# Kernel tuning notes

Hardware: AMD Instinct MI355X
Metric: run time of the kernel (lower is better)

The kernel has to match this reference:

```python
import jax, jax.numpy as jnp
import numpy as np

EMBED_DIM = 1024  # scaling uses embedding_dim**-0.5, as in the source
NEG_INF = -1e9    # keras Softmax masking constant


def setup_inputs() -> dict:
    key = jax.random.key(0)
    k0, k1, k2, k3 = jax.random.split(key, 4)
    B, S, D, H = 8, 2048, 1024, 128
    x = jax.random.normal(k0, (B, S, D), dtype=jnp.float32)
    Wq = jax.random.normal(k1, (D, H), dtype=jnp.float32) * (D ** -0.5)
    Wk = jax.random.normal(k2, (D, H), dtype=jnp.float32) * (D ** -0.5)
    Wv = jax.random.normal(k3, (D, H), dtype=jnp.float32) * (D ** -0.5)
    return {"x": x, "Wq": Wq, "Wk": Wk, "Wv": Wv}


def reference(x, Wq, Wk, Wv):
    # bias-free projections: [B,S,D] @ [D,H] -> [B,S,H]
    q = jnp.einsum("bsd,dh->bsh", x, Wq)
    k = jnp.einsum("bsd,dh->bsh", x, Wk)
    v = jnp.einsum("bsd,dh->bsh", x, Wv)
    # raw scores scaled by embedding_dim**-0.5 (faithful to source)
    w = jnp.einsum("bqh,bkh->bqk", q, k) * (EMBED_DIM ** -0.5)  # [B,S,S]
    # mask = bool(band_part(w, -1, 0)): lower triangle where score != 0
    S = w.shape[-1]
    tril = jnp.tril(jnp.ones((S, S), dtype=bool))
    mask = tril & (w != 0)
    # keras Softmax with mask: add -1e9 where mask is False, then softmax
    w = jnp.where(mask, w, NEG_INF)
    attn = jax.nn.softmax(w, axis=-1)
    return jnp.einsum("bqk,bkh->bqh", attn, v)
```

## Files before the change

kernel.cpp:

```cpp
#include <hip/hip_runtime.h>

typedef short bf8 __attribute__((ext_vector_type(8)));
typedef float f32x4 __attribute__((ext_vector_type(4)));
typedef unsigned short ushort;
typedef unsigned int uint;

#define MFMA16(a, b, c) __builtin_amdgcn_mfma_f32_16x16x32_bf16((a), (b), (c), 0, 0, 0)

static __device__ __forceinline__ ushort f2bf(float f) {
    union { float f; uint u; } v; v.f = f;
    uint u = v.u + 0x7FFFu + ((v.u >> 16) & 1u);
    return (ushort)(u >> 16);
}
static __device__ __forceinline__ float bf2f(ushort u) {
    union { uint u; float f; } v; v.u = ((uint)u) << 16; return v.f;
}
static __device__ __forceinline__ uint pk2(float a, float b) {
    return (uint)f2bf(a) | ((uint)f2bf(b) << 16);
}
static __device__ __forceinline__ void gload16(const void* g, void* l) {
    __builtin_amdgcn_global_load_lds((const __attribute__((address_space(1))) void*)g,
                                     (__attribute__((address_space(3))) void*)l, 16, 0, 0);
}

__global__ __launch_bounds__(256) void k_wconvert(const float* __restrict__ Wq,
                                                  const float* __restrict__ Wk,
                                                  const float* __restrict__ Wv,
                                                  ushort* __restrict__ wT) {
    int idx  = blockIdx.x * 256 + threadIdx.x;
    int proj = idx >> 14;
    int kc   = (idx >> 7) & 127;
    int n    = idx & 127;
    const float* W = (proj == 0) ? Wq : (proj == 1 ? Wk : Wv);
    uint4 w;
    float f[8];
#pragma unroll
    for (int j = 0; j < 8; ++j) f[j] = W[(kc * 8 + j) * 128 + n];
    w.x = pk2(f[0], f[1]); w.y = pk2(f[2], f[3]);
    w.z = pk2(f[4], f[5]); w.w = pk2(f[6], f[7]);
    *(uint4*)&wT[(size_t)proj * 131072 + (size_t)n * 1024 + kc * 8] = w;
}

__global__ __launch_bounds__(256, 3) void k_proj(const float* __restrict__ x,
                                                 const ushort* __restrict__ wT,
                                                 ushort* __restrict__ qb,
                                                 ushort* __restrict__ kb,
                                                 ushort* __restrict__ vT) {
    const int bx = blockIdx.x;
    const int mt = bx & 255;
    const int proj = bx >> 8;
    const int tid = threadIdx.x, lane = tid & 63, wid = tid >> 6;
    const int wm = wid >> 1, wn = wid & 1;
    const int m0 = mt * 64;

    __shared__ __align__(16) ushort sm[64 * 64 + 128 * 64];
    ushort* lA = sm;
    ushort* lB = sm + 64 * 64;

    const ushort* wTp = wT + (size_t)proj * 131072;
    f32x4 acc[2][4] = {};

    const int arow = tid >> 2, aq = tid & 3;
    const float* xrow = x + (size_t)(m0 + arow) * 1024 + aq * 16;

    for (int kt = 0; kt < 1024; kt += 64) {
        __syncthreads();
#pragma unroll
        for (int c = 0; c < 4; ++c) {
            int chunk = tid + 256 * c;
            int n = chunk >> 3, ir = (chunk & 7) * 8;
            gload16(wTp + (size_t)n * 1024 + kt + (ir ^ ((n & 7) << 3)),
                    lB + (size_t)(wid * 64 + 256 * c) * 8);
        }
        {
            const float* xs = xrow + kt;
            float4 a0 = *(const float4*)(xs);
            float4 a1 = *(const float4*)(xs + 4);
            float4 a2 = *(const float4*)(xs + 8);
            float4 a3 = *(const float4*)(xs + 12);
            uint4 w0, w1;
            w0.x = pk2(a0.x, a0.y); w0.y = pk2(a0.z, a0.w);
            w0.z = pk2(a1.x, a1.y); w0.w = pk2(a1.z, a1.w);
            w1.x = pk2(a2.x, a2.y); w1.y = pk2(a2.z, a2.w);
            w1.z = pk2(a3.x, a3.y); w1.w = pk2(a3.z, a3.w);
            const int swz = (arow & 7) << 3;
            const int ir0 = aq * 16;
            *(uint4*)&lA[arow * 64 + (ir0 ^ swz)] = w0;
            *(uint4*)&lA[arow * 64 + ((ir0 + 8) ^ swz)] = w1;
        }
        __syncthreads();

#pragma unroll
        for (int kk = 0; kk < 2; ++kk) {
            const int ir = kk * 32 + (lane >> 4) * 8;
            bf8 a[2], bv[4];
#pragma unroll
            for (int mf = 0; mf < 2; ++mf) {
                int r = wm * 32 + mf * 16 + (lane & 15);
                a[mf] = *(const bf8*)&lA[r * 64 + (ir ^ ((r & 7) << 3))];
            }
#pragma unroll
            for (int nf = 0; nf < 4; ++nf) {
                int r = wn * 64 + nf * 16 + (lane & 15);
                bv[nf] = *(const bf8*)&lB[r * 64 + (ir ^ ((r & 7) << 3))];
            }
#pragma unroll
            for (int mf = 0; mf < 2; ++mf)
#pragma unroll
                for (int nf = 0; nf < 4; ++nf)
                    acc[mf][nf] = MFMA16(a[mf], bv[nf], acc[mf][nf]);
        }
    }
    __syncthreads();

    if (proj < 2) {
        ushort* lT = sm;
#pragma unroll
        for (int mf = 0; mf < 2; ++mf) {
            int row = wm * 32 + mf * 16 + ((lane >> 4) << 2);
#pragma unroll
            for (int nf = 0; nf < 4; ++nf) {
                int col = wn * 64 + nf * 16 + (lane & 15);
#pragma unroll
                for (int i = 0; i < 4; ++i)
                    lT[(row + i) * 136 + col] = f2bf(acc[mf][nf][i]);
            }
        }
        __syncthreads();
        const int row = tid >> 2, seg = (tid & 3) * 32;
        ushort* dst = (proj == 0 ? qb : kb) + (size_t)(m0 + row) * 128 + seg;
        const ushort* srcr = lT + row * 136 + seg;
#pragma unroll
        for (int j = 0; j < 4; ++j)
            *(uint4*)&dst[j * 8] = *(const uint4*)&srcr[j * 8];
    } else {
        ushort* lT = sm;
#pragma unroll
        for (int mf = 0; mf < 2; ++mf) {
            int srow = wm * 32 + mf * 16 + ((lane >> 4) << 2);
#pragma unroll
            for (int nf = 0; nf < 4; ++nf) {
                int h = wn * 64 + nf * 16 + (lane & 15);
#pragma unroll
                for (int i = 0; i < 4; ++i)
                    lT[h * 72 + srow + i] = f2bf(acc[mf][nf][i]);
            }
        }
        __syncthreads();
        const int b = m0 >> 11, s0 = m0 & 2047;
        const int h = tid >> 1, so = (tid & 1) * 32;
        ushort* dst = vT + (size_t)b * 262144 + (size_t)h * 2048 + s0 + so;
#pragma unroll
        for (int j = 0; j < 4; ++j)
            *(uint4*)&dst[j * 8] = *(const uint4*)&lT[h * 72 + so + j * 8];
    }
}

#define NCHUNK 144

__global__ __launch_bounds__(256) void k_attn_part(const ushort* __restrict__ qb,
                                                   const ushort* __restrict__ kb,
                                                   const ushort* __restrict__ vT,
                                                   ushort* __restrict__ pacc,
                                                   float* __restrict__ pml) {
    const int id = blockIdx.x;
    const int b  = id & 7;
    const int cx = 143 - (id >> 3);
    int g = 0, base = 0;
#pragma unroll
    for (int gg = 0; gg < 8; ++gg) {
        int b0 = 2 * gg * (gg + 1);
        if (cx >= b0) { g = gg; base = b0; }
    }
    const int qt = 4 * g + (cx - base) / (g + 1);
    const int c  = (cx - base) % (g + 1);
    const int kt0 = 4 * c;
    const int kt1 = min(qt + 1, kt0 + 4);

    const int tid = threadIdx.x, lane = tid & 63, wid = tid >> 6;

    __shared__ __align__(16) ushort lK[64 * 128];
    __shared__ __align__(16) ushort lV[128 * 64];
    __shared__ __align__(16) ushort lP[4][16 * 64];

    bf8 qf[4];
    {
        const ushort* qr = qb + (size_t)(b * 2048 + qt * 64 + wid * 16 + (lane & 15)) * 128;
#pragma unroll
        for (int kk = 0; kk < 4; ++kk)
            qf[kk] = *(const bf8*)&qr[kk * 32 + (lane >> 4) * 8];
    }
    bf8 onesf;
#pragma unroll
    for (int j = 0; j < 8; ++j) onesf[j] = (short)0x3F80;

    f32x4 acc[8] = {};
    f32x4 accl = {};
    const int r0 = wid * 16 + ((lane >> 4) << 2);
    const int qg0 = qt * 64 + r0;

    const ushort* kbase = kb + (size_t)b * 2048 * 128;
    const ushort* vbase = vT + (size_t)b * 262144;

    for (int kt = kt0; kt < kt1; ++kt) {
        __syncthreads();
        {
            const ushort* kbt = kbase + (size_t)kt * 64 * 128;
#pragma unroll
            for (int cc = 0; cc < 4; ++cc) {
                int chunk = tid + 256 * cc;
                int rr = chunk >> 4, ir = (chunk & 15) * 8;
                gload16(kbt + (size_t)rr * 128 + (ir ^ ((rr & 7) << 3)),
                        lK + (size_t)(wid * 64 + 256 * cc) * 8);
            }
        }
        {
            const ushort* vbt = vbase + kt * 64;
#pragma unroll
            for (int cc = 0; cc < 4; ++cc) {
                int chunk = tid + 256 * cc;
                int h = chunk >> 3, ir = (chunk & 7) * 8;
                gload16(vbt + (size_t)h * 2048 + (ir ^ ((h & 7) << 3)),
                        lV + (size_t)(wid * 64 + 256 * cc) * 8);
            }
        }
        __syncthreads();

        f32x4 sa[4] = {};
#pragma unroll
        for (int kk = 0; kk < 4; ++kk) {
            const int ir = kk * 32 + (lane >> 4) * 8;
#pragma unroll
            for (int nf = 0; nf < 4; ++nf) {
                int rr = nf * 16 + (lane & 15);
                bf8 kf = *(const bf8*)&lK[rr * 128 + (ir ^ ((rr & 7) << 3))];
                sa[nf] = MFMA16(qf[kk], kf, sa[nf]);
            }
        }

        float p[4][4];
#pragma unroll
        for (int nf = 0; nf < 4; ++nf)
#pragma unroll
            for (int i = 0; i < 4; ++i) {
                float s = sa[nf][i] * 0.03125f;
                if (kt == qt) {
                    int kg = kt * 64 + nf * 16 + (lane & 15);
                    if (kg > qg0 + i) s = -1e30f;
                }
                p[nf][i] = __expf(s);
            }

#pragma unroll
        for (int nf = 0; nf < 4; ++nf)
#pragma unroll
            for (int i = 0; i < 4; ++i) {
                int rr = ((lane >> 4) << 2) + i, cp = nf * 16 + (lane & 15);
                lP[wid][rr * 64 + (cp ^ ((rr & 7) << 3))] = f2bf(p[nf][i]);
            }

#pragma unroll
        for (int kk = 0; kk < 2; ++kk) {
            const int ir = kk * 32 + (lane >> 4) * 8;
            const int pr = lane & 15;
            bf8 pf = *(const bf8*)&lP[wid][pr * 64 + (ir ^ ((pr & 7) << 3))];
            accl = MFMA16(pf, onesf, accl);
#pragma unroll
            for (int nf = 0; nf < 8; ++nf) {
                int h = nf * 16 + (lane & 15);
                bf8 vf = *(const bf8*)&lV[h * 64 + (ir ^ ((h & 7) << 3))];
                acc[nf] = MFMA16(pf, vf, acc[nf]);
            }
        }
    }

    ushort* pa = pacc + ((size_t)(b * NCHUNK + cx) * 64) * 128;
#pragma unroll
    for (int nf = 0; nf < 8; ++nf) {
        int h = nf * 16 + (lane & 15);
#pragma unroll
        for (int i = 0; i < 4; ++i)
            pa[(size_t)(r0 + i) * 128 + h] = f2bf(acc[nf][i]);
    }
    if ((lane & 15) == 0) {
        float* pl = pml + (size_t)(b * NCHUNK + cx) * 64 + r0;
#pragma unroll
        for (int i = 0; i < 4; ++i) pl[i] = accl[i];
    }
}

__global__ __launch_bounds__(256) void k_attn_comb(const ushort* __restrict__ pacc,
                                                   const float* __restrict__ pml,
                                                   float* __restrict__ out) {
    const int qt = blockIdx.x, b = blockIdx.y, z = blockIdx.z;
    const int tid = threadIdx.x;
    const int row = tid >> 2, cq = ((tid & 3) + 4 * z) * 16;
    const int g = qt >> 2;
    const int base = 2 * g * (g + 1) + (qt & 3) * (g + 1);
    const int nch = g + 1;

    float L = 0.f;
    for (int c = 0; c < nch; ++c)
        L += pml[(size_t)(b * NCHUNK + base + c) * 64 + row];
    const float inv = 1.0f / L;

    float s[16] = {};
    for (int c = 0; c < nch; ++c) {
        const ushort* pa = pacc + ((size_t)(b * NCHUNK + base + c) * 64 + row) * 128 + cq;
#pragma unroll
        for (int j = 0; j < 2; ++j) {
            uint4 t = *(const uint4*)&pa[j * 8];
            uint qw[4] = {t.x, t.y, t.z, t.w};
#pragma unroll
            for (int e = 0; e < 4; ++e) {
                s[j * 8 + 2 * e]     += bf2f((ushort)(qw[e] & 0xFFFFu));
                s[j * 8 + 2 * e + 1] += bf2f((ushort)(qw[e] >> 16));
            }
        }
    }
    float* o = out + ((size_t)(b * 2048 + qt * 64 + row)) * 128 + cq;
#pragma unroll
    for (int j = 0; j < 4; ++j) {
        f32x4 v;
#pragma unroll
        for (int e = 0; e < 4; ++e) v[e] = s[j * 4 + e] * inv;
        *(f32x4*)&o[j * 4] = v;
    }
}

extern "C" void kernel_launch(void* const* d_in, const int* in_sizes, int n_in,
                              void* d_out, int out_size, void* d_ws, size_t ws_size,
                              hipStream_t stream) {
    const float* x  = (const float*)d_in[0];
    const float* Wq = (const float*)d_in[1];
    const float* Wk = (const float*)d_in[2];
    const float* Wv = (const float*)d_in[3];
    float* out = (float*)d_out;

    char* ws = (char*)d_ws;
    ushort* qb = (ushort*)(ws);
    ushort* kb = (ushort*)(ws + (4u << 20));
    ushort* vT = (ushort*)(ws + (8u << 20));
    ushort* wT = (ushort*)(ws + (12u << 20));
    float*  pml  = (float*)(ws + (13u << 20));
    ushort* pacc = (ushort*)(ws + (15u << 20));

    k_wconvert<<<192, 256, 0, stream>>>(Wq, Wk, Wv, wT);
    k_proj<<<768, 256, 0, stream>>>(x, wT, qb, kb, vT);
    k_attn_part<<<NCHUNK * 8, 256, 0, stream>>>(qb, kb, vT, pacc, pml);
    k_attn_comb<<<dim3(32, 8, 2), 256, 0, stream>>>(pacc, pml, out);
}
```

Before: 68.93 us.

## Enlarge attention query tile to 128 rows with 512-thread blocks

Doubles the query rows per attention-partial block from 64 to 128 by running eight waves per block. Each K/V tile loaded into LDS is then shared by twice as many query rows, which halves K/V global traffic and the chunk count. The chunk schedule, causal masking, partial-buffer indexing and combine kernel are rewritten for the new tiling. In exchange there are fewer blocks (576 instead of 1152), so parallelism drops, and more masked work is wasted on the diagonal tiles.

```diff
diff --git a/kernel.cpp b/kernel.cpp
--- a/kernel.cpp
+++ b/kernel.cpp
@@ -156,36 +156,37 @@
     }
 }
 
-#define NCHUNK 144
-
-__global__ __launch_bounds__(256) void k_attn_part(const ushort* __restrict__ qb,
+#define NCHUNK 72
+
+__global__ __launch_bounds__(512) void k_attn_part(const ushort* __restrict__ qb,
                                                    const ushort* __restrict__ kb,
                                                    const ushort* __restrict__ vT,
                                                    ushort* __restrict__ pacc,
                                                    float* __restrict__ pml) {
     const int id = blockIdx.x;
     const int b  = id & 7;
-    const int cx = 143 - (id >> 3);
-    int g = 0, base = 0;
-#pragma unroll
-    for (int gg = 0; gg < 8; ++gg) {
-        int b0 = 2 * gg * (gg + 1);
-        if (cx >= b0) { g = gg; base = b0; }
-    }
-    const int qt = 4 * g + (cx - base) / (g + 1);
-    const int c  = (cx - base) % (g + 1);
+    const int cx = 71 - (id >> 3);
+    int h = 0, base = 0;
+#pragma unroll
+    for (int hh = 0; hh < 8; ++hh) {
+        int b0 = hh * (hh + 1);
+        if (cx >= b0) { h = hh; base = b0; }
+    }
+    const int rem = cx - base;
+    const int qt = 2 * h + rem / (h + 1);
+    const int c  = rem % (h + 1);
     const int kt0 = 4 * c;
-    const int kt1 = min(qt + 1, kt0 + 4);
+    const int kt1 = min(2 * qt + 2, kt0 + 4);
 
     const int tid = threadIdx.x, lane = tid & 63, wid = tid >> 6;
 
     __shared__ __align__(16) ushort lK[64 * 128];
     __shared__ __align__(16) ushort lV[128 * 64];
-    __shared__ __align__(16) ushort lP[4][16 * 64];
+    __shared__ __align__(16) ushort lP[8][16 * 64];
 
     bf8 qf[4];
     {
-        const ushort* qr = qb + (size_t)(b * 2048 + qt * 64 + wid * 16 + (lane & 15)) * 128;
+        const ushort* qr = qb + (size_t)(b * 2048 + qt * 128 + wid * 16 + (lane & 15)) * 128;
 #pragma unroll
         for (int kk = 0; kk < 4; ++kk)
             qf[kk] = *(const bf8*)&qr[kk * 32 + (lane >> 4) * 8];
@@ -197,7 +198,7 @@
     f32x4 acc[8] = {};
     f32x4 accl = {};
     const int r0 = wid * 16 + ((lane >> 4) << 2);
-    const int qg0 = qt * 64 + r0;
+    const int qg0 = qt * 128 + r0;
 
     const ushort* kbase = kb + (size_t)b * 2048 * 128;
     const ushort* vbase = vT + (size_t)b * 262144;
@@ -207,21 +208,21 @@
         {
             const ushort* kbt = kbase + (size_t)kt * 64 * 128;
 #pragma unroll
-            for (int cc = 0; cc < 4; ++cc) {
-                int chunk = tid + 256 * cc;
+            for (int cc = 0; cc < 2; ++cc) {
+                int chunk = tid + 512 * cc;
                 int rr = chunk >> 4, ir = (chunk & 15) * 8;
                 gload16(kbt + (size_t)rr * 128 + (ir ^ ((rr & 7) << 3)),
-                        lK + (size_t)(wid * 64 + 256 * cc) * 8);
+                        lK + (size_t)(wid * 64 + 512 * cc) * 8);
             }
         }
         {
             const ushort* vbt = vbase + kt * 64;
 #pragma unroll
-            for (int cc = 0; cc < 4; ++cc) {
-                int chunk = tid + 256 * cc;
-                int h = chunk >> 3, ir = (chunk & 7) * 8;
-                gload16(vbt + (size_t)h * 2048 + (ir ^ ((h & 7) << 3)),
-                        lV + (size_t)(wid * 64 + 256 * cc) * 8);
+            for (int cc = 0; cc < 2; ++cc) {
+                int chunk = tid + 512 * cc;
+                int hh = chunk >> 3, ir = (chunk & 7) * 8;
+                gload16(vbt + (size_t)hh * 2048 + (ir ^ ((hh & 7) << 3)),
+                        lV + (size_t)(wid * 64 + 512 * cc) * 8);
             }
         }
         __syncthreads();
@@ -244,7 +245,7 @@
 #pragma unroll
             for (int i = 0; i < 4; ++i) {
                 float s = sa[nf][i] * 0.03125f;
-                if (kt == qt) {
+                if (kt >= 2 * qt) {
                     int kg = kt * 64 + nf * 16 + (lane & 15);
                     if (kg > qg0 + i) s = -1e30f;
                 }
@@ -267,23 +268,23 @@
             accl = MFMA16(pf, onesf, accl);
 #pragma unroll
             for (int nf = 0; nf < 8; ++nf) {
-                int h = nf * 16 + (lane & 15);
-                bf8 vf = *(const bf8*)&lV[h * 64 + (ir ^ ((h & 7) << 3))];
+                int hh = nf * 16 + (lane & 15);
+                bf8 vf = *(const bf8*)&lV[hh * 64 + (ir ^ ((hh & 7) << 3))];
                 acc[nf] = MFMA16(pf, vf, acc[nf]);
             }
         }
     }
 
-    ushort* pa = pacc + ((size_t)(b * NCHUNK + cx) * 64) * 128;
+    ushort* pa = pacc + ((size_t)(b * NCHUNK + cx) * 128) * 128;
 #pragma unroll
     for (int nf = 0; nf < 8; ++nf) {
-        int h = nf * 16 + (lane & 15);
+        int hh = nf * 16 + (lane & 15);
 #pragma unroll
         for (int i = 0; i < 4; ++i)
-            pa[(size_t)(r0 + i) * 128 + h] = f2bf(acc[nf][i]);
+            pa[(size_t)(r0 + i) * 128 + hh] = f2bf(acc[nf][i]);
     }
     if ((lane & 15) == 0) {
-        float* pl = pml + (size_t)(b * NCHUNK + cx) * 64 + r0;
+        float* pl = pml + (size_t)(b * NCHUNK + cx) * 128 + r0;
 #pragma unroll
         for (int i = 0; i < 4; ++i) pl[i] = accl[i];
     }
@@ -294,19 +295,19 @@
                                                    float* __restrict__ out) {
     const int qt = blockIdx.x, b = blockIdx.y, z = blockIdx.z;
     const int tid = threadIdx.x;
-    const int row = tid >> 2, cq = ((tid & 3) + 4 * z) * 16;
-    const int g = qt >> 2;
-    const int base = 2 * g * (g + 1) + (qt & 3) * (g + 1);
-    const int nch = g + 1;
+    const int row = tid >> 1, cq = ((tid & 1) + 2 * z) * 16;
+    const int h = qt >> 1;
+    const int base = h * (h + 1) + (qt & 1) * (h + 1);
+    const int nch = h + 1;
 
     float L = 0.f;
     for (int c = 0; c < nch; ++c)
-        L += pml[(size_t)(b * NCHUNK + base + c) * 64 + row];
+        L += pml[(size_t)(b * NCHUNK + base + c) * 128 + row];
     const float inv = 1.0f / L;
 
     float s[16] = {};
     for (int c = 0; c < nch; ++c) {
-        const ushort* pa = pacc + ((size_t)(b * NCHUNK + base + c) * 64 + row) * 128 + cq;
+        const ushort* pa = pacc + ((size_t)(b * NCHUNK + base + c) * 128 + row) * 128 + cq;
 #pragma unroll
         for (int j = 0; j < 2; ++j) {
             uint4 t = *(const uint4*)&pa[j * 8];
@@ -318,7 +319,7 @@
             }
         }
     }
-    float* o = out + ((size_t)(b * 2048 + qt * 64 + row)) * 128 + cq;
+    float* o = out + ((size_t)(b * 2048 + qt * 128 + row)) * 128 + cq;
 #pragma unroll
     for (int j = 0; j < 4; ++j) {
         f32x4 v;
@@ -347,6 +348,6 @@
 
     k_wconvert<<<192, 256, 0, stream>>>(Wq, Wk, Wv, wT);
     k_proj<<<768, 256, 0, stream>>>(x, wT, qb, kb, vT);
-    k_attn_part<<<NCHUNK * 8, 256, 0, stream>>>(qb, kb, vT, pacc, pml);
-    k_attn_comb<<<dim3(32, 8, 2), 256, 0, stream>>>(pacc, pml, out);
-}
+    k_attn_part<<<NCHUNK * 8, 512, 0, stream>>>(qb, kb, vT, pacc, pml);
+    k_attn_comb<<<dim3(16, 8, 4), 256, 0, stream>>>(pacc, pml, out);
+}
```

New measurement: 73.93 us. 1.07x slower.
